# Kernel tuning notes

Hardware: AMD Instinct MI355X
Metric: run time of the kernel (lower is better)

The kernel has to match this reference:

```python
import jax, jax.numpy as jnp
import numpy as np

N_NODES = 1536
IN_FEATURES = 1433
N_HIDDEN = 64      # total across 8 heads -> 8 per head
N_HEADS = 8
N_CLASSES = 7
NEG_SLOPE = 0.2    # LeakyReLU slope in GATv2 layer


def setup_inputs() -> dict:
    key = jax.random.key(0)
    k_x, k_adj, k_w1, k_a1, k_w2, k_a2 = jax.random.split(key, 6)
    x = jax.random.normal(k_x, (N_NODES, IN_FEATURES), dtype=jnp.float32)
    adj = jax.random.uniform(k_adj, (N_NODES, N_NODES)) < 0.01
    adj = adj | jnp.eye(N_NODES, dtype=bool)
    adj_mat = adj[:, :, None]  # [n, n, 1]
    # layer 1 (share_weights=True -> one linear for l and r), attn vector shared across heads
    s1 = 1.0 / np.sqrt(IN_FEATURES)
    W1 = jax.random.uniform(k_w1, (IN_FEATURES, N_HIDDEN), minval=-s1, maxval=s1, dtype=jnp.float32)
    a1 = jax.random.uniform(k_a1, (N_HIDDEN // N_HEADS,), minval=-1.0, maxval=1.0, dtype=jnp.float32)
    # layer 2: 1 head, n_classes features, is_concat=False (mean over the single head)
    s2 = 1.0 / np.sqrt(N_HIDDEN)
    W2 = jax.random.uniform(k_w2, (N_HIDDEN, N_CLASSES), minval=-s2, maxval=s2, dtype=jnp.float32)
    a2 = jax.random.uniform(k_a2, (N_CLASSES,), minval=-1.0, maxval=1.0, dtype=jnp.float32)
    return {"x": x, "adj_mat": adj_mat, "W1": W1, "a1": a1, "W2": W2, "a2": a2}


def _gatv2_layer(h, adj, W, a, n_heads, is_concat):
    n = h.shape[0]
    g = (h @ W).reshape(n, n_heads, -1)              # shared weights: g_l == g_r == g
    # pairwise scores: e[i,j,h] = a . leaky_relu(g[j] + g[i])  (symmetric since weights shared)
    s = jax.nn.leaky_relu(g[:, None] + g[None, :], NEG_SLOPE)   # [n, n, heads, f]
    e = jnp.einsum('ijhf,f->ijh', s, a)                          # [n, n, heads]
    e = jnp.where(adj, e, -jnp.inf)                              # adj broadcasts [n,n,1]
    att = jax.nn.softmax(e, axis=1)                              # softmax over source nodes j
    out = jnp.einsum('ijh,jhf->ihf', att, g)                     # [n, heads, f]
    if is_concat:
        return out.reshape(n, -1)
    return out.mean(axis=1)


def reference(x, adj_mat, W1, a1, W2, a2):
    # dropout layers are identity in eval mode
    h = _gatv2_layer(x, adj_mat, W1, a1, N_HEADS, True)   # [n, n_hidden]
    h = jax.nn.elu(h)
    return _gatv2_layer(h, adj_mat, W2, a2, 1, False)     # [n, n_classes]
```

## Files before the change

### kernel.cpp

```cpp
#include <hip/hip_runtime.h>

#define N_NODES 1536
#define IN_F    1433
#define HID     64
#define NH      8
#define HF      8
#define NC      7
#define MAXN    64
#define GST     66
#define G1_BLOCKS 384
#define ROWS    4
#define XS_STRIDE 1440

__device__ __forceinline__ float waveAllMax(float v) {
#pragma unroll
    for (int o = 32; o > 0; o >>= 1) v = fmaxf(v, __shfl_xor(v, o, 64));
    return v;
}
__device__ __forceinline__ float waveAllSum(float v) {
#pragma unroll
    for (int o = 32; o > 0; o >>= 1) v += __shfl_xor(v, o, 64);
    return v;
}

__global__ __launch_bounds__(256) void k_front(const float* __restrict__ x,
                                               const float* __restrict__ W1,
                                               const unsigned int* __restrict__ adj,
                                               float* __restrict__ g1,
                                               int* __restrict__ cnt,
                                               int* __restrict__ nbr) {
    __shared__ float xs[ROWS * XS_STRIDE];
    __shared__ float red[4 * 256];
    __shared__ int lc;
    const int t = threadIdx.x;

    if (blockIdx.x < G1_BLOCKS) {
        const int i0 = blockIdx.x * ROWS;
        for (int r = 0; r < ROWS; ++r) {
            const float* xr = x + (size_t)(i0 + r) * IN_F;
            for (int k = t; k < XS_STRIDE; k += 256)
                xs[r * XS_STRIDE + k] = (k < IN_F) ? xr[k] : 0.f;
        }
        __syncthreads();
        const int j = t & 63, q = t >> 6;
        float acc[ROWS] = {0.f, 0.f, 0.f, 0.f};
        const int k0 = q * 360;
        for (int kb = k0; kb < k0 + 360; kb += 4) {
            float w[4];
#pragma unroll
            for (int u = 0; u < 4; ++u) {
                int k = kb + u;
                int kc = (k < IN_F) ? k : (IN_F - 1);
                w[u] = W1[(size_t)kc * HID + j];
            }
#pragma unroll
            for (int r = 0; r < ROWS; ++r) {
                float4 xv = *(const float4*)(xs + r * XS_STRIDE + kb);
                acc[r] += xv.x * w[0] + xv.y * w[1] + xv.z * w[2] + xv.w * w[3];
            }
        }
#pragma unroll
        for (int r = 0; r < ROWS; ++r) red[q * 256 + r * 64 + j] = acc[r];
        __syncthreads();
        float s = red[0 * 256 + t] + red[1 * 256 + t] + red[2 * 256 + t] + red[3 * 256 + t];
        g1[(size_t)(i0 + (t >> 6)) * HID + (t & 63)] = s;
    } else {
        const int i = blockIdx.x - G1_BLOCKS;
        if (t == 0) lc = 0;
        __syncthreads();
        const unsigned int* row = adj + (size_t)i * N_NODES;
        for (int j = t; j < N_NODES; j += 256) {
            if (row[j] != 0u) {
                int p = atomicAdd(&lc, 1);
                if (p < MAXN) nbr[i * MAXN + p] = j;
            }
        }
        __syncthreads();
        if (t == 0) {
            int n = (lc > MAXN) ? MAXN : lc;
            if (n == 0) { nbr[i * MAXN] = i; n = 1; }
            cnt[i] = n;
        }
    }
}

__global__ __launch_bounds__(64) void k_attn1(const float* __restrict__ g1,
                                              const int* __restrict__ cnt,
                                              const int* __restrict__ nbr,
                                              const float* __restrict__ a1,
                                              float* __restrict__ h1) {
    __shared__ float gis[HID];
    __shared__ float gj[MAXN * GST];
    __shared__ float es[NH * GST];
    const int i = blockIdx.x, t = threadIdx.x;
    const int n = cnt[i];

    gis[t] = g1[(size_t)i * HID + t];
    const int jn = nbr[i * MAXN + t];
    for (int l = 0; l < n; ++l) {
        int j = __shfl(jn, l, 64);
        gj[l * GST + t] = g1[(size_t)j * HID + t];
    }
    __syncthreads();

    float av[HF];
#pragma unroll
    for (int f = 0; f < HF; ++f) av[f] = a1[f];

    float sc[NH];
    if (t < n) {
#pragma unroll
        for (int h = 0; h < NH; ++h) {
            float s = 0.f;
#pragma unroll
            for (int f = 0; f < HF; ++f) {
                float v = gis[h * HF + f] + gj[t * GST + h * HF + f];
                v = (v >= 0.f) ? v : 0.2f * v;
                s += av[f] * v;
            }
            sc[h] = s;
        }
    } else {
#pragma unroll
        for (int h = 0; h < NH; ++h) sc[h] = -INFINITY;
    }

    float S[NH];
#pragma unroll
    for (int h = 0; h < NH; ++h) {
        float m = waveAllMax(sc[h]);
        float p = (t < n) ? __expf(sc[h] - m) : 0.f;
        es[h * GST + t] = p;
        S[h] = waveAllSum(p);
    }
    __syncthreads();

    const int h = t >> 3;
    float acc = 0.f;
    for (int l = 0; l < n; ++l)
        acc += es[h * GST + l] * gj[l * GST + t];
    acc /= S[h];
    h1[(size_t)i * HID + t] = (acc > 0.f) ? acc : (__expf(acc) - 1.f);
}

__global__ __launch_bounds__(64) void k_back(const float* __restrict__ h1,
                                             const float* __restrict__ W2,
                                             const float* __restrict__ a2,
                                             const int* __restrict__ cnt,
                                             const int* __restrict__ nbr,
                                             float* __restrict__ out) {
    __shared__ float hj[MAXN * GST];
    __shared__ float w2s[HID * NC];
    __shared__ float g2s[MAXN * 8];
    __shared__ float ps[MAXN];
    const int i = blockIdx.x, t = threadIdx.x;
    const int n = cnt[i];

    for (int k = t; k < HID * NC; k += 64) w2s[k] = W2[k];
    const int jn = nbr[i * MAXN + t];
    for (int l = 0; l < n; ++l) {
        int j = __shfl(jn, l, 64);
        hj[l * GST + t] = h1[(size_t)j * HID + t];
    }
    __syncthreads();

    if (t < n) {
#pragma unroll
        for (int c = 0; c < NC; ++c) {
            float s = 0.f;
            for (int f = 0; f < HID; ++f)
                s += hj[t * GST + f] * w2s[f * NC + c];
            g2s[t * 8 + c] = s;
        }
    }
    unsigned long long bal = __ballot(t < n && jn == i);
    int ls = (bal != 0ull) ? (__ffsll((long long)bal) - 1) : 0;
    __syncthreads();

    float scv;
    if (t < n) {
        float s = 0.f;
#pragma unroll
        for (int c = 0; c < NC; ++c) {
            float v = g2s[ls * 8 + c] + g2s[t * 8 + c];
            v = (v >= 0.f) ? v : 0.2f * v;
            s += a2[c] * v;
        }
        scv = s;
    } else scv = -INFINITY;

    float m = waveAllMax(scv);
    float p = (t < n) ? __expf(scv - m) : 0.f;
    ps[t] = p;
    float S = waveAllSum(p);
    __syncthreads();

    if (t < NC) {
        float acc = 0.f;
        for (int l = 0; l < n; ++l)
            acc += ps[l] * g2s[l * 8 + t];
        out[(size_t)i * NC + t] = acc / S;
    }
}

extern "C" void kernel_launch(void* const* d_in, const int* in_sizes, int n_in,
                              void* d_out, int out_size, void* d_ws, size_t ws_size,
                              hipStream_t stream) {
    (void)out_size; (void)ws_size;
    const void* px = nullptr; const void* padj = nullptr;
    const void* pW1 = nullptr; const void* pa1 = nullptr;
    const void* pW2 = nullptr; const void* pa2 = nullptr;
    for (int i = 0; i < n_in; ++i) {
        switch (in_sizes[i]) {
            case N_NODES * IN_F:    px   = d_in[i]; break;
            case N_NODES * N_NODES: padj = d_in[i]; break;
            case IN_F * HID:        pW1  = d_in[i]; break;
            case HF:                pa1  = d_in[i]; break;
            case HID * NC:          pW2  = d_in[i]; break;
            case NC:                pa2  = d_in[i]; break;
            default: break;
        }
    }
    if (!px && n_in > 0)   px   = d_in[0];
    if (!padj && n_in > 1) padj = d_in[1];
    if (!pW1 && n_in > 2)  pW1  = d_in[2];
    if (!pa1 && n_in > 3)  pa1  = d_in[3];
    if (!pW2 && n_in > 4)  pW2  = d_in[4];
    if (!pa2 && n_in > 5)  pa2  = d_in[5];

    char* w = (char*)d_ws;
    size_t off = 0;
    auto carve = [&](size_t bytes) -> char* {
        off = (off + 255) & ~(size_t)255;
        char* p = w + off; off += bytes; return p;
    };
    int*   cnt = (int*)  carve((size_t)N_NODES * 4);
    int*   nbr = (int*)  carve((size_t)N_NODES * MAXN * 4);
    float* g1  = (float*)carve((size_t)N_NODES * HID * 4);
    float* h1  = (float*)carve((size_t)N_NODES * HID * 4);

    float* outp = (float*)d_out;

    k_front<<<G1_BLOCKS + N_NODES, 256, 0, stream>>>((const float*)px, (const float*)pW1,
                                                     (const unsigned int*)padj, g1, cnt, nbr);
    k_attn1<<<N_NODES, 64, 0, stream>>>(g1, cnt, nbr, (const float*)pa1, h1);
    k_back<<<N_NODES, 64, 0, stream>>>(h1, (const float*)pW2, (const float*)pa2,
                                       cnt, nbr, outp);
}
```

Measured before the change: 123.1 us.

## Split attention and output kernels across two waves with batched neighbor gathers

Launches the per-node attention kernels with two wavefronts instead of one. Neighbor rows are gathered four at a time, interleaved across waves, to expose more memory-level parallelism. Heads (layer 1) and output classes (layer 2) are divided between the waves, and the layer-1 aggregation is split over neighbors and combined with a shuffle. This adds idle threads in the small layer-2 softmax stage and relies on per-wave ownership of shared arrays to avoid extra barriers.

```diff
diff --git a/kernel.cpp b/kernel.cpp
--- a/kernel.cpp
+++ b/kernel.cpp
@@ -84,22 +84,33 @@
     }
 }
 
-__global__ __launch_bounds__(64) void k_attn1(const float* __restrict__ g1,
-                                              const int* __restrict__ cnt,
-                                              const int* __restrict__ nbr,
-                                              const float* __restrict__ a1,
-                                              float* __restrict__ h1) {
+__global__ __launch_bounds__(128) void k_attn1(const float* __restrict__ g1,
+                                               const int* __restrict__ cnt,
+                                               const int* __restrict__ nbr,
+                                               const float* __restrict__ a1,
+                                               float* __restrict__ h1) {
     __shared__ float gis[HID];
     __shared__ float gj[MAXN * GST];
     __shared__ float es[NH * GST];
-    const int i = blockIdx.x, t = threadIdx.x;
+    const int i = blockIdx.x, tid = threadIdx.x;
+    const int t = tid & 63, w = tid >> 6;
     const int n = cnt[i];
 
-    gis[t] = g1[(size_t)i * HID + t];
+    if (tid < HID) gis[tid] = g1[(size_t)i * HID + tid];
     const int jn = nbr[i * MAXN + t];
-    for (int l = 0; l < n; ++l) {
-        int j = __shfl(jn, l, 64);
-        gj[l * GST + t] = g1[(size_t)j * HID + t];
+
+    for (int l0 = 4 * w; l0 < n; l0 += 8) {
+        float v[4];
+#pragma unroll
+        for (int u = 0; u < 4; ++u) {
+            int l = l0 + u;
+            int lc = (l < n) ? l : (n - 1);
+            int j = __shfl(jn, lc, 64);
+            v[u] = g1[(size_t)j * HID + t];
+        }
+#pragma unroll
+        for (int u = 0; u < 4; ++u)
+            if (l0 + u < n) gj[(l0 + u) * GST + t] = v[u];
     }
     __syncthreads();
 
@@ -107,10 +118,11 @@
 #pragma unroll
     for (int f = 0; f < HF; ++f) av[f] = a1[f];
 
-    float sc[NH];
+    float sc[4];
     if (t < n) {
 #pragma unroll
-        for (int h = 0; h < NH; ++h) {
+        for (int hh = 0; hh < 4; ++hh) {
+            const int h = 4 * w + hh;
             float s = 0.f;
 #pragma unroll
             for (int f = 0; f < HF; ++f) {
@@ -118,56 +130,68 @@
                 v = (v >= 0.f) ? v : 0.2f * v;
                 s += av[f] * v;
             }
-            sc[h] = s;
+            sc[hh] = s;
         }
     } else {
 #pragma unroll
-        for (int h = 0; h < NH; ++h) sc[h] = -INFINITY;
-    }
-
-    float S[NH];
-#pragma unroll
-    for (int h = 0; h < NH; ++h) {
-        float m = waveAllMax(sc[h]);
-        float p = (t < n) ? __expf(sc[h] - m) : 0.f;
-        es[h * GST + t] = p;
-        S[h] = waveAllSum(p);
-    }
-    __syncthreads();
-
-    const int h = t >> 3;
+        for (int hh = 0; hh < 4; ++hh) sc[hh] = -INFINITY;
+    }
+
+#pragma unroll
+    for (int hh = 0; hh < 4; ++hh) {
+        const int h = 4 * w + hh;
+        float m = waveAllMax(sc[hh]);
+        float p = (t < n) ? __expf(sc[hh] - m) : 0.f;
+        float S = waveAllSum(p);
+        es[h * GST + t] = p / S;
+    }
+
+    const int c = 32 * w + (t & 31);
+    const int h = c >> 3;
     float acc = 0.f;
-    for (int l = 0; l < n; ++l)
-        acc += es[h * GST + l] * gj[l * GST + t];
-    acc /= S[h];
-    h1[(size_t)i * HID + t] = (acc > 0.f) ? acc : (__expf(acc) - 1.f);
-}
-
-__global__ __launch_bounds__(64) void k_back(const float* __restrict__ h1,
-                                             const float* __restrict__ W2,
-                                             const float* __restrict__ a2,
-                                             const int* __restrict__ cnt,
-                                             const int* __restrict__ nbr,
-                                             float* __restrict__ out) {
+    for (int l = (t >> 5); l < n; l += 2)
+        acc += es[h * GST + l] * gj[l * GST + c];
+    acc += __shfl_xor(acc, 32, 64);
+    if (t < 32)
+        h1[(size_t)i * HID + c] = (acc > 0.f) ? acc : (__expf(acc) - 1.f);
+}
+
+__global__ __launch_bounds__(128) void k_back(const float* __restrict__ h1,
+                                              const float* __restrict__ W2,
+                                              const float* __restrict__ a2,
+                                              const int* __restrict__ cnt,
+                                              const int* __restrict__ nbr,
+                                              float* __restrict__ out) {
     __shared__ float hj[MAXN * GST];
     __shared__ float w2s[HID * NC];
     __shared__ float g2s[MAXN * 8];
     __shared__ float ps[MAXN];
-    const int i = blockIdx.x, t = threadIdx.x;
+    const int i = blockIdx.x, tid = threadIdx.x;
+    const int t = tid & 63, w = tid >> 6;
     const int n = cnt[i];
 
-    for (int k = t; k < HID * NC; k += 64) w2s[k] = W2[k];
+    for (int k = tid; k < HID * NC; k += 128) w2s[k] = W2[k];
     const int jn = nbr[i * MAXN + t];
-    for (int l = 0; l < n; ++l) {
-        int j = __shfl(jn, l, 64);
-        hj[l * GST + t] = h1[(size_t)j * HID + t];
+    for (int l0 = 4 * w; l0 < n; l0 += 8) {
+        float v[4];
+#pragma unroll
+        for (int u = 0; u < 4; ++u) {
+            int l = l0 + u;
+            int lc = (l < n) ? l : (n - 1);
+            int j = __shfl(jn, lc, 64);
+            v[u] = h1[(size_t)j * HID + t];
+        }
+#pragma unroll
+        for (int u = 0; u < 4; ++u)
+            if (l0 + u < n) hj[(l0 + u) * GST + t] = v[u];
     }
     __syncthreads();
 
     if (t < n) {
-#pragma unroll
-        for (int c = 0; c < NC; ++c) {
+        const int c0 = 4 * w, c1 = (w == 0) ? 4 : 7;
+        for (int c = c0; c < c1; ++c) {
             float s = 0.f;
+#pragma unroll
             for (int f = 0; f < HID; ++f)
                 s += hj[t * GST + f] * w2s[f * NC + c];
             g2s[t * 8 + c] = s;
@@ -177,29 +201,30 @@
     int ls = (bal != 0ull) ? (__ffsll((long long)bal) - 1) : 0;
     __syncthreads();
 
-    float scv;
-    if (t < n) {
-        float s = 0.f;
-#pragma unroll
-        for (int c = 0; c < NC; ++c) {
-            float v = g2s[ls * 8 + c] + g2s[t * 8 + c];
-            v = (v >= 0.f) ? v : 0.2f * v;
-            s += a2[c] * v;
-        }
-        scv = s;
-    } else scv = -INFINITY;
-
-    float m = waveAllMax(scv);
-    float p = (t < n) ? __expf(scv - m) : 0.f;
-    ps[t] = p;
-    float S = waveAllSum(p);
-    __syncthreads();
-
-    if (t < NC) {
-        float acc = 0.f;
-        for (int l = 0; l < n; ++l)
-            acc += ps[l] * g2s[l * 8 + t];
-        out[(size_t)i * NC + t] = acc / S;
+    if (w == 0) {
+        float scv;
+        if (t < n) {
+            float s = 0.f;
+#pragma unroll
+            for (int c = 0; c < NC; ++c) {
+                float v = g2s[ls * 8 + c] + g2s[t * 8 + c];
+                v = (v >= 0.f) ? v : 0.2f * v;
+                s += a2[c] * v;
+            }
+            scv = s;
+        } else scv = -INFINITY;
+
+        float m = waveAllMax(scv);
+        float p = (t < n) ? __expf(scv - m) : 0.f;
+        ps[t] = p;
+        float S = waveAllSum(p);
+
+        if (t < NC) {
+            float acc = 0.f;
+            for (int l = 0; l < n; ++l)
+                acc += ps[l] * g2s[l * 8 + t];
+            out[(size_t)i * NC + t] = acc / S;
+        }
     }
 }
 
@@ -243,7 +268,7 @@
 
     k_front<<<G1_BLOCKS + N_NODES, 256, 0, stream>>>((const float*)px, (const float*)pW1,
                                                      (const unsigned int*)padj, g1, cnt, nbr);
-    k_attn1<<<N_NODES, 64, 0, stream>>>(g1, cnt, nbr, (const float*)pa1, h1);
-    k_back<<<N_NODES, 64, 0, stream>>>(h1, (const float*)pW2, (const float*)pa2,
-                                       cnt, nbr, outp);
-}
+    k_attn1<<<N_NODES, 128, 0, stream>>>(g1, cnt, nbr, (const float*)pa1, h1);
+    k_back<<<N_NODES, 128, 0, stream>>>(h1, (const float*)pW2, (const float*)pa2,
+                                        cnt, nbr, outp);
+}
```

Measured after the change: 115.0 us. -6.6%, faster.
